# Optimization experiments

Hardware: AMD Instinct MI355X
Metric: run time of the kernel (lower is better)

The kernel has to match this reference:

```python
import jax, jax.numpy as jnp
import numpy as np
from jax import lax

B, D, H, N = 2048, 256, 256, 64  # batch, input_dim, hidden_dim, n_slots
F = 2 * D + 1                    # feat_dim = input_dim*2 + 1


def setup_inputs() -> dict:
    key = jax.random.key(0)
    ks = jax.random.split(key, 12)
    s = 0.05
    return {
        "x_t": jax.random.normal(ks[0], (B, D), jnp.float32),
        "h_mem_prev": jnp.zeros((B, H), jnp.float32),
        "slots": jax.random.normal(ks[1], (B, N, D), jnp.float32),
        "cum_feats": jax.random.normal(ks[2], (B, N, D), jnp.float32),
        "delta_t": jax.random.uniform(ks[3], (B, N), jnp.float32),
        "filled": jax.random.randint(ks[4], (B, N), 0, 2) > 0,
        # nn.Linear weights (out, in) convention
        "Wq": jax.random.normal(ks[5], (H, D), jnp.float32) * s,
        "Wk": jax.random.normal(ks[6], (H, D), jnp.float32) * s,
        "Wv": jax.random.normal(ks[7], (D, D), jnp.float32) * s,
        "bv": jax.random.normal(ks[8], (D,), jnp.float32) * s,
        # nn.LSTM params, gate order [i, f, g, o]
        "W_ih": jax.random.normal(ks[9], (4 * H, F), jnp.float32) * s,
        "W_hh": jax.random.normal(ks[10], (4 * H, H), jnp.float32) * s,
        "b_ih": jax.random.normal(ks[11], (4 * H,), jnp.float32) * s,
        "b_hh": jnp.zeros((4 * H,), jnp.float32),
    }


def _lstm_last(seq, W_ih, W_hh, b_ih, b_hh):
    """seq: (B, T, F) -> last hidden output (B, H). PyTorch gate order i,f,g,o."""
    Bsz = seq.shape[0]
    Hh = W_hh.shape[1]
    b = b_ih + b_hh

    def step(carry, x_t):
        h, c = carry
        z = x_t @ W_ih.T + h @ W_hh.T + b  # (B, 4H)
        i, f, g, o = jnp.split(z, 4, axis=-1)
        c = jax.nn.sigmoid(f) * c + jax.nn.sigmoid(i) * jnp.tanh(g)
        h = jax.nn.sigmoid(o) * jnp.tanh(c)
        return (h, c), None

    init = (jnp.zeros((Bsz, Hh), seq.dtype), jnp.zeros((Bsz, Hh), seq.dtype))
    (h, _), _ = lax.scan(step, init, jnp.swapaxes(seq, 0, 1))
    return h


def reference(x_t, h_mem_prev, slots, cum_feats, delta_t, filled,
              Wq, Wk, Wv, bv, W_ih, W_hh, b_ih, b_hh):
    Bsz = x_t.shape[0]
    delta_t = delta_t + 1.0
    cum_feats = cum_feats + x_t[:, None, :]

    q = x_t @ Wq.T                          # (B, H)
    keys = jnp.einsum('bnd,hd->bnh', slots, Wk)
    sims = jnp.einsum('bnh,bh->bn', keys, q)

    v = x_t @ Wv.T + bv                     # (B, D)

    empty = ~filled
    empty_any = empty.any(axis=1)
    idx_empty = jnp.argmax(empty.astype(jnp.float32), axis=1)
    idx_cont = jnp.argmax(sims, axis=1)
    idx = jnp.where(empty_any, idx_empty, idx_cont)  # (B,) int

    ar = jnp.arange(Bsz)
    slots = slots.at[ar, idx].set(v)
    cum_feats = cum_feats.at[ar, idx].set(x_t)
    delta_t = delta_t.at[ar, idx].set(0.0)
    filled = filled.at[ar, idx].set(True)

    mem_seq = jnp.concatenate([slots, cum_feats, delta_t[..., None]], axis=2)  # (B, N, F)
    h_mem = _lstm_last(mem_seq, W_ih, W_hh, b_ih, b_hh)
    return h_mem, slots, cum_feats, delta_t, filled
```

## Files before the change

kernel.cpp:

```cpp
#include <hip/hip_runtime.h>
#include <hip/hip_bf16.h>
#include <cstdint>
#include <cstddef>


typedef short s16x8 __attribute__((ext_vector_type(8)));
typedef float f32x4 __attribute__((ext_vector_type(4)));
typedef int   i32x4 __attribute__((ext_vector_type(4)));

static __device__ __forceinline__ unsigned short f2b(float f){
  union{float f; unsigned int u;} v; v.f = f;
  unsigned int r = v.u + 0x7fffu + ((v.u >> 16) & 1u);
  return (unsigned short)(r >> 16);
}
static __device__ __forceinline__ float b2f(unsigned short h){
  union{unsigned int u; float f;} v; v.u = ((unsigned int)h) << 16; return v.f;
}
static __device__ __forceinline__ unsigned int pack2(float a, float b){
  return (unsigned int)f2b(a) | ((unsigned int)f2b(b) << 16);
}
static __device__ __forceinline__ float fsig(float x){ return 1.0f / (1.0f + __expf(-x)); }
static __device__ __forceinline__ float ftanh(float x){ return 2.0f / (1.0f + __expf(-2.0f * x)) - 1.0f; }
static __device__ __forceinline__ float wred(float p){
  p += __shfl_down(p, 32); p += __shfl_down(p, 16); p += __shfl_down(p, 8);
  p += __shfl_down(p, 4);  p += __shfl_down(p, 2);  p += __shfl_down(p, 1);
  return p;
}
static __device__ __forceinline__ void gload16(const void* g, void* lds){
  __builtin_amdgcn_global_load_lds(
      (const __attribute__((address_space(1))) unsigned int*)g,
      (__attribute__((address_space(3))) unsigned int*)lds, 16, 0, 0);
}

#define WSCALE (0.30f / 127.0f)

__global__ __launch_bounds__(256) void k_prep(
    const float* __restrict__ wih, const float* __restrict__ whh,
    const float* __restrict__ bih, const float* __restrict__ bhh,
    unsigned short* __restrict__ wfB, signed char* __restrict__ wfrag8,
    float* __restrict__ bias, float* __restrict__ wlast){
  int id = blockIdx.x * 256 + threadIdx.x;
  {
    int frag = id >> 9;
    int l = (id >> 3) & 63;
    int j = id & 7;
    int kt = frag >> 6, ct = frag & 63;
    int col = ct * 16 + (l & 15);
    int k   = kt * 32 + (l >> 4) * 8 + j;
    wfB[id] = f2b(wih[col * 513 + k]);
  }
  if (id < 262144){
    int frag = id >> 9;
    int lane = (id >> 3) & 63;
    int j    = id & 7;
    int w  = frag >> 6;
    int kt = (frag >> 3) & 7;
    int nt = frag & 7;
    int g  = nt >> 1, hh = nt & 1;
    int colg = g * 256 + w * 32 + hh * 16 + (lane & 15);
    int k    = kt * 32 + (lane >> 4) * 8 + j;
    int q = __float2int_rn(whh[colg * 256 + k] * (1.0f / WSCALE));
    q = q > 127 ? 127 : (q < -127 ? -127 : q);
    wfrag8[frag * 512 + lane * 8 + j] = (signed char)q;
  }
  if (id < 1024){
    bias[id]  = bih[id] + bhh[id];
    wlast[id] = wih[id * 513 + 512];
  }
}

__global__ __launch_bounds__(256) void k_route(
    const float* __restrict__ x, const float* __restrict__ slots,
    const float* __restrict__ delta, const int* __restrict__ filled,
    const float* __restrict__ Wq, const float* __restrict__ Wk,
    const float* __restrict__ Wv, const float* __restrict__ bv,
    int* __restrict__ idx_ws, float* __restrict__ v_ws,
    float* __restrict__ delta_out, float* __restrict__ filled_out){
  int b = blockIdx.x, tid = threadIdx.x, l = tid & 63, w = tid >> 6;
  __shared__ float xs[256], qs[256], qks[256], sims[64];
  __shared__ int sidx;
  xs[tid] = x[b * 256 + tid];
  if (tid < 64){
    unsigned long long em = __ballot(filled[b * 64 + tid] == 0);
    if (tid == 0) sidx = em ? (int)__builtin_ctzll(em) : -1;
  }
  __syncthreads();
  for (int t = 0; t < 64; ++t){
    int h = w * 64 + t;
    float pv = 0.f;
    #pragma unroll
    for (int j2 = 0; j2 < 4; ++j2)
      pv += Wv[h * 256 + l + 64 * j2] * xs[l + 64 * j2];
    pv = wred(pv);
    if (l == 0) v_ws[b * 256 + h] = pv + bv[h];
  }
  if (sidx < 0){
    for (int t = 0; t < 64; ++t){
      int h = w * 64 + t;
      float p = 0.f;
      #pragma unroll
      for (int j2 = 0; j2 < 4; ++j2)
        p += Wq[h * 256 + l + 64 * j2] * xs[l + 64 * j2];
      p = wred(p);
      if (l == 0) qs[h] = p;
    }
    __syncthreads();
    {
      int d = tid; float p = 0.f;
      for (int h = 0; h < 256; ++h) p += qs[h] * Wk[h * 256 + d];
      qks[d] = p;
    }
    __syncthreads();
    for (int t = 0; t < 16; ++t){
      int n = w * 16 + t;
      float p = 0.f;
      #pragma unroll
      for (int j2 = 0; j2 < 4; ++j2)
        p += slots[(size_t)(b * 64 + n) * 256 + l + 64 * j2] * qks[l + 64 * j2];
      p = wred(p);
      if (l == 0) sims[n] = p;
    }
    __syncthreads();
    if (tid == 0){
      int ic = 0; float best = sims[0];
      for (int n = 1; n < 64; ++n) if (sims[n] > best){ best = sims[n]; ic = n; }
      sidx = ic;
    }
  }
  __syncthreads();
  int id = sidx;
  if (tid == 0) idx_ws[b] = id;
  if (tid < 64){
    int n = tid; bool sel = (n == id);
    delta_out[b * 64 + n]  = sel ? 0.0f : (delta[b * 64 + n] + 1.0f);
    filled_out[b * 64 + n] = (sel || filled[b * 64 + n] != 0) ? 1.0f : 0.0f;
  }
}

__global__ __launch_bounds__(256) void k_scatter(
    const float* __restrict__ x, const float* __restrict__ slots,
    const float* __restrict__ cum, const int* __restrict__ idx_ws,
    const float* __restrict__ v_ws,
    float* __restrict__ slots_out, float* __restrict__ cum_out,
    unsigned short* __restrict__ abf){
  int rg = threadIdx.x >> 6, l = threadIdx.x & 63;
  int row = blockIdx.x * 4 + rg;
  int b = row >> 6, n = row & 63;
  bool sel = (n == idx_ws[b]);
  float4 f0, f1;
  if (l < 32){
    int k0 = l * 8;
    const float* src = sel ? (v_ws + (size_t)b * 256 + k0)
                           : (slots + (size_t)row * 256 + k0);
    f0 = ((const float4*)src)[0]; f1 = ((const float4*)src)[1];
    float4* d = (float4*)(slots_out + (size_t)row * 256 + k0);
    d[0] = f0; d[1] = f1;
  } else {
    int k0 = (l - 32) * 8;
    const float4* xp = (const float4*)(x + (size_t)b * 256 + k0);
    float4 x0 = xp[0], x1 = xp[1];
    if (sel){ f0 = x0; f1 = x1; }
    else {
      const float4* cp = (const float4*)(cum + (size_t)row * 256 + k0);
      f0 = cp[0]; f1 = cp[1];
      f0.x += x0.x; f0.y += x0.y; f0.z += x0.z; f0.w += x0.w;
      f1.x += x1.x; f1.y += x1.y; f1.z += x1.z; f1.w += x1.w;
    }
    float4* d = (float4*)(cum_out + (size_t)row * 256 + k0);
    d[0] = f0; d[1] = f1;
  }
  uint4 q;
  q.x = pack2(f0.x, f0.y); q.y = pack2(f0.z, f0.w);
  q.z = pack2(f1.x, f1.y); q.w = pack2(f1.z, f1.w);
  *(uint4*)(abf + (size_t)row * 512 + l * 8) = q;
}

__global__ __launch_bounds__(512) void k_gemm(
    const unsigned short* __restrict__ abf,
    const float* __restrict__ dlt,
    const unsigned short* __restrict__ wfB,
    const float* __restrict__ wlast, const float* __restrict__ bias,
    unsigned short* __restrict__ z0){
  extern __shared__ unsigned char L[];
  int tid = threadIdx.x, l = tid & 63, w = tid >> 6;
  int bid = blockIdx.x;
  int gw = (bid & 7) * 512 + (bid >> 3);
  int n_idx = gw & 3, m_idx = gw >> 2;
  int m0 = m_idx * 128, n0 = n_idx * 256, bA = m0 >> 6;
  int wm = w & 1, wn = w >> 1;
  int cl = l & 15, lhi = l >> 4;

  auto stageA = [&](int kt, int abase){
    const unsigned short* s = abf + (size_t)(m0 + (w & 1) * 64 + l) * 512
                              + kt * 32 + (w >> 1) * 8;
    gload16(s, L + abase + (w >> 1) * 2048 + (w & 1) * 1024);
  };
  auto stageB = [&](int kt, int bbase){
    const unsigned short* s = wfB + ((size_t)(kt * 64 + n_idx * 16 + w * 2)) * 512 + l * 8;
    gload16(s,       L + bbase + (w * 2) * 1024);
    gload16(s + 512, L + bbase + (w * 2) * 1024 + 1024);
  };

  f32x4 acc[4][4];
  #pragma unroll
  for (int mi = 0; mi < 4; ++mi)
    #pragma unroll
    for (int ni = 0; ni < 4; ++ni){ f32x4 zr = {0.f,0.f,0.f,0.f}; acc[mi][ni] = zr; }

  stageA(0, 0);      stageB(0, 24576);
  stageA(1, 8192);   stageB(1, 24576 + 16384);

  #pragma unroll
  for (int kt = 0; kt < 16; ++kt){
    if (kt < 14){
      int nb = (kt + 2) % 3;
      stageA(kt + 2, nb * 8192);
      stageB(kt + 2, 24576 + nb * 16384);
    }
    if (kt < 14)       asm volatile("s_waitcnt vmcnt(6)" ::: "memory");
    else if (kt == 14) asm volatile("s_waitcnt vmcnt(3)" ::: "memory");
    else               asm volatile("s_waitcnt vmcnt(0)" ::: "memory");
    __builtin_amdgcn_s_barrier();
    __builtin_amdgcn_sched_barrier(0);
    int ab = (kt % 3) * 8192, bb = 24576 + (kt % 3) * 16384;
    s16x8 a[4], bf[4];
    #pragma unroll
    for (int mi = 0; mi < 4; ++mi)
      a[mi] = *(const s16x8*)(L + ab + lhi * 2048 + (wm * 64 + mi * 16 + cl) * 16);
    #pragma unroll
    for (int ni = 0; ni < 4; ++ni)
      bf[ni] = *(const s16x8*)(L + bb + (wn * 4 + ni) * 1024 + l * 16);
    #pragma unroll
    for (int ni = 0; ni < 4; ++ni)
      #pragma unroll
      for (int mi = 0; mi < 4; ++mi)
        acc[mi][ni] = __builtin_amdgcn_mfma_f32_16x16x32_bf16(a[mi], bf[ni], acc[mi][ni], 0, 0, 0);
    __builtin_amdgcn_sched_barrier(0);
    __builtin_amdgcn_s_barrier();
  }

  float dv[4][4];
  #pragma unroll
  for (int mi = 0; mi < 4; ++mi)
    #pragma unroll
    for (int reg = 0; reg < 4; ++reg)
      dv[mi][reg] = dlt[(bA + wm) * 64 + mi * 16 + lhi * 4 + reg];
  #pragma unroll
  for (int mi = 0; mi < 4; ++mi)
    #pragma unroll
    for (int reg = 0; reg < 4; ++reg){
      int row = wm * 64 + mi * 16 + lhi * 4 + reg;
      #pragma unroll
      for (int ni = 0; ni < 4; ++ni){
        int col = wn * 64 + ni * 16 + cl;
        int gc = n0 + col;
        float val = acc[mi][ni][reg] + dv[mi][reg] * wlast[gc] + bias[gc];
        *(unsigned short*)(L + row * 512 + ((col * 2) ^ ((row & 7) << 4))) = f2b(val);
      }
    }
  __syncthreads();
  #pragma unroll
  for (int rr = 0; rr < 8; ++rr){
    int id = rr * 512 + tid;
    int row = id >> 5, cs = id & 31;
    int bq = bA + (row >> 6), nq = row & 63;
    uint4 v = *(const uint4*)(L + row * 512 + ((cs * 16) ^ ((row & 7) << 4)));
    *(uint4*)(z0 + ((size_t)nq * 2048 + bq) * 1024 + n0 + cs * 8) = v;
  }
}

__global__ __launch_bounds__(512) void k_lstm(
    const unsigned short* __restrict__ z0,
    const signed char* __restrict__ wfrag8,
    float* __restrict__ hm){
  extern __shared__ unsigned char smem[];
  unsigned char* zbuf = smem;
  unsigned char* zhh  = smem + 32768;
  unsigned char* hbf  = smem + 65536;
  int tid = threadIdx.x, l = tid & 63, w = tid >> 6;
  int cl = l & 15, lhi = l >> 4;
  int b0 = blockIdx.x * 8;

  for (int i = tid; i < 1024; i += 512) ((unsigned int*)hbf)[i] = 0u;

  long long wpin[64];
  #pragma unroll
  for (int f = 0; f < 64; ++f)
    wpin[f] = *(const long long*)(wfrag8 + ((size_t)w * 64 + f) * 512 + l * 8);

  {
    const uint4* src = (const uint4*)(z0 + (size_t)b0 * 1024);
    int rr = tid >> 6, off = (tid & 63) * 32;
    unsigned char* base = zbuf + rr * 2048;
    *(uint4*)(base + ((off)      ^ ((rr & 7) << 4))) = src[tid * 2];
    *(uint4*)(base + ((off + 16) ^ ((rr & 7) << 4))) = src[tid * 2 + 1];
  }
  float cst[4];
  #pragma unroll
  for (int i = 0; i < 4; ++i) cst[i] = 0.f;
  const float s_comb = WSCALE / 127.0f;
  __syncthreads();

  for (int n = 0; n < 64; ++n){
    uint4 zp0, zp1;
    if (n < 63){
      const uint4* src = (const uint4*)(z0 + ((size_t)(n + 1) * 2048 + b0) * 1024);
      zp0 = src[tid * 2]; zp1 = src[tid * 2 + 1];
    }
    i32x4 acc[8];
    #pragma unroll
    for (int nt = 0; nt < 8; ++nt){ i32x4 zr = {0, 0, 0, 0}; acc[nt] = zr; }
    #pragma unroll
    for (int kt = 0; kt < 8; ++kt){
      int byteo = cl * 256 + ((kt * 32 + lhi * 8) ^ ((cl & 7) << 3));
      long long a = *(const long long*)(hbf + byteo);
      #pragma unroll
      for (int nt = 0; nt < 8; ++nt)
        acc[nt] = __builtin_amdgcn_mfma_i32_16x16x32_i8(a, wpin[kt * 8 + nt], acc[nt], 0, 0, 0);
    }
    if (n < 63){
      int rr = tid >> 6, off = (tid & 63) * 32;
      unsigned char* base = zbuf + ((n + 1) & 1) * 16384 + rr * 2048;
      *(uint4*)(base + ((off)      ^ ((rr & 7) << 4))) = zp0;
      *(uint4*)(base + ((off + 16) ^ ((rr & 7) << 4))) = zp1;
    }
    if (l < 32){
      #pragma unroll
      for (int hh = 0; hh < 2; ++hh){
        int ch = w * 32 + hh * 16 + cl;
        #pragma unroll
        for (int reg = 0; reg < 4; ++reg){
          int rr = lhi * 4 + reg;
          float4 v;
          v.x = (float)acc[0 + hh][reg];
          v.y = (float)acc[2 + hh][reg];
          v.z = (float)acc[4 + hh][reg];
          v.w = (float)acc[6 + hh][reg];
          *(float4*)(zhh + (rr * 256 + ch) * 16) = v;
        }
      }
    }
    __syncthreads();
    const unsigned char* zc = zbuf + (n & 1) * 16384;
    #pragma unroll
    for (int i = 0; i < 4; ++i){
      int id = tid + i * 512;
      int rr = id >> 8, ch = id & 255;
      float4 a4 = *(const float4*)(zhh + id * 16);
      const unsigned char* zr = zc + rr * 2048;
      int sw = (rr & 7) << 4;
      float zi = fmaf(a4.x, s_comb, b2f(*(const unsigned short*)(zr + (((0 * 256 + ch) * 2) ^ sw))));
      float zf = fmaf(a4.y, s_comb, b2f(*(const unsigned short*)(zr + (((1 * 256 + ch) * 2) ^ sw))));
      float zg = fmaf(a4.z, s_comb, b2f(*(const unsigned short*)(zr + (((2 * 256 + ch) * 2) ^ sw))));
      float zo = fmaf(a4.w, s_comb, b2f(*(const unsigned short*)(zr + (((3 * 256 + ch) * 2) ^ sw))));
      float cv = fsig(zf) * cst[i] + fsig(zi) * ftanh(zg);
      cst[i] = cv;
      float hv = fsig(zo) * ftanh(cv);
      hbf[rr * 256 + (ch ^ ((rr & 7) << 3))] = (signed char)__float2int_rn(hv * 127.0f);
      if (n == 63) hm[(size_t)(b0 + rr) * 256 + ch] = hv;
    }
    __syncthreads();
  }
}

extern "C" void kernel_launch(void* const* d_in, const int* in_sizes, int n_in,
                              void* d_out, int out_size, void* d_ws, size_t ws_size,
                              hipStream_t stream){
  const float* x      = (const float*)d_in[0];
  const float* slots  = (const float*)d_in[2];
  const float* cum    = (const float*)d_in[3];
  const float* delta  = (const float*)d_in[4];
  const int*   filled = (const int*)d_in[5];
  const float* Wq  = (const float*)d_in[6];
  const float* Wk  = (const float*)d_in[7];
  const float* Wv  = (const float*)d_in[8];
  const float* bv  = (const float*)d_in[9];
  const float* wih = (const float*)d_in[10];
  const float* whh = (const float*)d_in[11];
  const float* bih = (const float*)d_in[12];
  const float* bhh = (const float*)d_in[13];

  float* out        = (float*)d_out;
  float* hm         = out;
  float* slots_out  = out + 524288;
  float* cum_out    = out + 34078720;
  float* delta_out  = out + 67633152;
  float* filled_out = out + 67764224;

  char* ws = (char*)d_ws;
  int*            idx_ws  = (int*)ws;
  float*          v_ws    = (float*)(ws + 8192);
  float*          bias    = (float*)(ws + 2105344);
  float*          wlast   = (float*)(ws + 2109440);
  unsigned short* wfB     = (unsigned short*)(ws + 2113536);
  signed char*    wfrag8  = (signed char*)(ws + 3162112);
  unsigned short* abf     = (unsigned short*)(ws + 3686400);
  unsigned short* z0      = (unsigned short*)(ws + 3686400 + 134217728);

  k_prep<<<dim3(2048), dim3(256), 0, stream>>>(wih, whh, bih, bhh, wfB, wfrag8, bias, wlast);
  k_route<<<dim3(2048), dim3(256), 0, stream>>>(x, slots, delta, filled, Wq, Wk, Wv, bv,
                                                idx_ws, v_ws, delta_out, filled_out);
  k_scatter<<<dim3(32768), dim3(256), 0, stream>>>(x, slots, cum, idx_ws, v_ws,
                                                   slots_out, cum_out, abf);
  k_gemm<<<dim3(4096), dim3(512), 73728, stream>>>(abf, delta_out,
                                                   wfB, wlast, bias, z0);
  k_lstm<<<dim3(256), dim3(512), 69632, stream>>>(z0, wfrag8, hm);
}
```

Before: 598.0 us.

## Halve LSTM batch rows per block to launch 512 blocks

```diff
diff --git a/kernel.cpp b/kernel.cpp
--- a/kernel.cpp
+++ b/kernel.cpp
@@ -275,88 +275,74 @@
     float* __restrict__ hm){
   extern __shared__ unsigned char smem[];
   unsigned char* zbuf = smem;
-  unsigned char* zhh  = smem + 32768;
-  unsigned char* hbf  = smem + 65536;
+  unsigned char* zhh  = smem + 16384;
+  unsigned char* hbf  = smem + 32768;
   int tid = threadIdx.x, l = tid & 63, w = tid >> 6;
   int cl = l & 15, lhi = l >> 4;
-  int b0 = blockIdx.x * 8;
-
-  for (int i = tid; i < 1024; i += 512) ((unsigned int*)hbf)[i] = 0u;
+  int b0 = blockIdx.x * 4;
+
+  if (tid < 256) ((unsigned int*)hbf)[tid] = 0u;
 
   long long wpin[64];
   #pragma unroll
   for (int f = 0; f < 64; ++f)
     wpin[f] = *(const long long*)(wfrag8 + ((size_t)w * 64 + f) * 512 + l * 8);
 
-  {
-    const uint4* src = (const uint4*)(z0 + (size_t)b0 * 1024);
-    int rr = tid >> 6, off = (tid & 63) * 32;
-    unsigned char* base = zbuf + rr * 2048;
-    *(uint4*)(base + ((off)      ^ ((rr & 7) << 4))) = src[tid * 2];
-    *(uint4*)(base + ((off + 16) ^ ((rr & 7) << 4))) = src[tid * 2 + 1];
-  }
-  float cst[4];
-  #pragma unroll
-  for (int i = 0; i < 4; ++i) cst[i] = 0.f;
+  ((uint4*)zbuf)[tid] = ((const uint4*)(z0 + (size_t)b0 * 1024))[tid];
+  float cst[2];
+  cst[0] = 0.f; cst[1] = 0.f;
   const float s_comb = WSCALE / 127.0f;
   __syncthreads();
 
   for (int n = 0; n < 64; ++n){
-    uint4 zp0, zp1;
-    if (n < 63){
-      const uint4* src = (const uint4*)(z0 + ((size_t)(n + 1) * 2048 + b0) * 1024);
-      zp0 = src[tid * 2]; zp1 = src[tid * 2 + 1];
-    }
+    uint4 zp;
+    if (n < 63)
+      zp = ((const uint4*)(z0 + ((size_t)(n + 1) * 2048 + b0) * 1024))[tid];
     i32x4 acc[8];
     #pragma unroll
     for (int nt = 0; nt < 8; ++nt){ i32x4 zr = {0, 0, 0, 0}; acc[nt] = zr; }
     #pragma unroll
     for (int kt = 0; kt < 8; ++kt){
-      int byteo = cl * 256 + ((kt * 32 + lhi * 8) ^ ((cl & 7) << 3));
-      long long a = *(const long long*)(hbf + byteo);
+      long long a = 0;
+      if (cl < 4)
+        a = *(const long long*)(hbf + cl * 256 + ((kt * 32 + lhi * 8) ^ ((cl & 3) << 3)));
       #pragma unroll
       for (int nt = 0; nt < 8; ++nt)
         acc[nt] = __builtin_amdgcn_mfma_i32_16x16x32_i8(a, wpin[kt * 8 + nt], acc[nt], 0, 0, 0);
     }
-    if (n < 63){
-      int rr = tid >> 6, off = (tid & 63) * 32;
-      unsigned char* base = zbuf + ((n + 1) & 1) * 16384 + rr * 2048;
-      *(uint4*)(base + ((off)      ^ ((rr & 7) << 4))) = zp0;
-      *(uint4*)(base + ((off + 16) ^ ((rr & 7) << 4))) = zp1;
-    }
-    if (l < 32){
+    if (n < 63)
+      ((uint4*)(zbuf + ((n + 1) & 1) * 8192))[tid] = zp;
+    if (l < 16){
       #pragma unroll
       for (int hh = 0; hh < 2; ++hh){
         int ch = w * 32 + hh * 16 + cl;
         #pragma unroll
         for (int reg = 0; reg < 4; ++reg){
-          int rr = lhi * 4 + reg;
           float4 v;
           v.x = (float)acc[0 + hh][reg];
           v.y = (float)acc[2 + hh][reg];
           v.z = (float)acc[4 + hh][reg];
           v.w = (float)acc[6 + hh][reg];
-          *(float4*)(zhh + (rr * 256 + ch) * 16) = v;
+          *(float4*)(zhh + (reg * 256 + ch) * 16) = v;
         }
       }
     }
     __syncthreads();
-    const unsigned char* zc = zbuf + (n & 1) * 16384;
-    #pragma unroll
-    for (int i = 0; i < 4; ++i){
+    const unsigned char* zc = zbuf + (n & 1) * 8192;
+    #pragma unroll
+    for (int i = 0; i < 2; ++i){
       int id = tid + i * 512;
       int rr = id >> 8, ch = id & 255;
       float4 a4 = *(const float4*)(zhh + id * 16);
-      const unsigned char* zr = zc + rr * 2048;
-      int sw = (rr & 7) << 4;
-      float zi = fmaf(a4.x, s_comb, b2f(*(const unsigned short*)(zr + (((0 * 256 + ch) * 2) ^ sw))));
-      float zf = fmaf(a4.y, s_comb, b2f(*(const unsigned short*)(zr + (((1 * 256 + ch) * 2) ^ sw))));
-      float zg = fmaf(a4.z, s_comb, b2f(*(const unsigned short*)(zr + (((2 * 256 + ch) * 2) ^ sw))));
-      float zo = fmaf(a4.w, s_comb, b2f(*(const unsigned short*)(zr + (((3 * 256 + ch) * 2) ^ sw))));
+      const unsigned short* zr = (const unsigned short*)(zc + rr * 2048);
+      float zi = fmaf(a4.x, s_comb, b2f(zr[0 * 256 + ch]));
+      float zf = fmaf(a4.y, s_comb, b2f(zr[1 * 256 + ch]));
+      float zg = fmaf(a4.z, s_comb, b2f(zr[2 * 256 + ch]));
+      float zo = fmaf(a4.w, s_comb, b2f(zr[3 * 256 + ch]));
       float cv = fsig(zf) * cst[i] + fsig(zi) * ftanh(zg);
       cst[i] = cv;
       float hv = fsig(zo) * ftanh(cv);
-      hbf[rr * 256 + (ch ^ ((rr & 7) << 3))] = (signed char)__float2int_rn(hv * 127.0f);
+      hbf[rr * 256 + (ch ^ ((rr & 3) << 3))] = (signed char)__float2int_rn(hv * 127.0f);
       if (n == 63) hm[(size_t)(b0 + rr) * 256 + ch] = hv;
     }
     __syncthreads();
@@ -404,5 +390,5 @@
                                                    slots_out, cum_out, abf);
   k_gemm<<<dim3(4096), dim3(512), 73728, stream>>>(abf, delta_out,
                                                    wfB, wlast, bias, z0);
-  k_lstm<<<dim3(256), dim3(512), 69632, stream>>>(z0, wfrag8, hm);
-}
+  k_lstm<<<dim3(512), dim3(512), 33792, stream>>>(z0, wfrag8, hm);
+}
```

New measurement: 665.0 us. +11.2%, slower.
